# Kernel optimization log

Hardware: AMD Instinct MI355X
Metric: run time of the kernel (lower is better)

## Reference

```python
import jax, jax.numpy as jnp
import numpy as np
from functools import partial

H, W = 96, 96                 # PNet output feature-map size
N = H * W                     # candidate boxes
STRIDE = 2.0
CELL = 12.0
SCALE = 12.0 / 20.0           # net_size / min_face_size (first pyramid level)
CLS_THR = 0.6
NMS_THR1 = 0.5                # per-scale NMS
NMS_THR2 = 0.7                # final NMS


def _iou_matrix(b):
    # b: [N,4] boxes (x1,y1,x2,y2); pixel convention with +1, eps as in source
    x1, y1, x2, y2 = b[:, 0], b[:, 1], b[:, 2], b[:, 3]
    area = (x2 - x1 + 1.0) * (y2 - y1 + 1.0)                      # [N]
    xx1 = jnp.maximum(x1[:, None], x1[None, :])
    yy1 = jnp.maximum(y1[:, None], y1[None, :])
    xx2 = jnp.minimum(x2[:, None], x2[None, :])
    yy2 = jnp.minimum(y2[:, None], y2[None, :])
    w = jnp.maximum(0.0, xx2 - xx1 + 1.0)
    h = jnp.maximum(0.0, yy2 - yy1 + 1.0)
    inter = w * h                                                  # [N,N]
    return inter / (area[:, None] + area[None, :] - inter + 1e-10)


def _greedy_nms(iou, valid, thr):
    # Sequential greedy suppression over score-sorted boxes (rows of iou).
    # A kept box suppresses all LOWER-ranked boxes with IoU > thr.
    n = valid.shape[0]
    ranks = jnp.arange(n)

    def step(suppressed, i):
        kept_i = valid[i] & (~suppressed[i])
        suppressed = suppressed | (kept_i & (iou[i] > thr) & (ranks > i))
        return suppressed, kept_i

    _, keep = jax.lax.scan(step, jnp.zeros(n, dtype=bool), ranks)
    return keep


def _forward(cls_map, reg):
    score = cls_map.reshape(-1)                                    # [N]
    dreg = reg.reshape(-1, 4)                                      # [N,4]
    ys, xs = jnp.meshgrid(jnp.arange(H, dtype=cls_map.dtype),
                          jnp.arange(W, dtype=cls_map.dtype), indexing='ij')
    x1 = jnp.round(STRIDE * xs / SCALE).reshape(-1)
    y1 = jnp.round(STRIDE * ys / SCALE).reshape(-1)
    x2 = jnp.round((STRIDE * xs + CELL) / SCALE).reshape(-1)
    y2 = jnp.round((STRIDE * ys + CELL) / SCALE).reshape(-1)
    boxes = jnp.stack([x1, y1, x2, y2], axis=1)                    # [N,4]

    order = jnp.argsort(-score)                                    # desc by score
    b = boxes[order]
    s = score[order]
    d = dreg[order]
    valid = s > CLS_THR                                            # threshold-gather as mask

    iou = _iou_matrix(b)                                           # [N,N] ~340MB
    keep = _greedy_nms(iou, valid, NMS_THR1)                       # per-scale NMS
    keep = _greedy_nms(iou, keep, NMS_THR2)                        # final NMS

    # box calibration (boxes_c in the source)
    bbw = b[:, 2] - b[:, 0] + 1.0
    bbh = b[:, 3] - b[:, 1] + 1.0
    boxes_c = jnp.stack([b[:, 0] + d[:, 0] * bbw,
                         b[:, 1] + d[:, 1] * bbh,
                         b[:, 2] + d[:, 2] * bbw,
                         b[:, 3] + d[:, 3] * bbh,
                         s], axis=1)                               # [N,5]
    return boxes_c * keep[:, None].astype(boxes_c.dtype)


def setup_inputs() -> dict:
    key = jax.random.key(0)
    k1, k2 = jax.random.split(key)
    cls_map = jax.random.uniform(k1, (H, W), dtype=jnp.float32)        # face prob channel
    reg = 0.1 * jax.random.normal(k2, (H, W, 4), dtype=jnp.float32)    # bbox offsets
    return {"cls_map": cls_map, "reg": reg}


def reference(cls_map, reg):
    return _forward(cls_map, reg)
```

## Files before the change

kernel.cpp:

```cpp
#include <hip/hip_runtime.h>
#include <stdint.h>

#define HH 96
#define WW 96
#define NN (HH*WW)
#define NW 192
#define NMT 24
#define MT 384
#define NKT 9


__device__ __forceinline__ int coord1(int a) { return (10 * a + 1) / 3; }

template<int H, int DJ>
__device__ __forceinline__ unsigned long long shf(unsigned long long S,
                                                  unsigned long long O) {
    if constexpr (DJ == 0) {
        return S;
    } else if constexpr (H == 0) {
        if constexpr (DJ > 0) return (S >> DJ) | (O << (64 - DJ));
        else                  return (S << (-DJ));
    } else {
        if constexpr (DJ > 0) return (S >> DJ);
        else                  return (S << (-DJ)) | (O >> (64 + DJ));
    }
}

template<int H>
__device__ __forceinline__ unsigned long long runfix(
    const int row, const unsigned long long (&Hr)[12],
    volatile unsigned long long* vKs, volatile unsigned long long* vKo,
    volatile unsigned long long* vDs, volatile unsigned long long* vDo,
    unsigned long long myK, unsigned long long myD) {
    const bool okm1 = row >= 1, okp1 = row <= HH - 2;
    const bool okm2 = row >= 2, okp2 = row <= HH - 3;
    for (int iter = 0; iter < 4096; ++iter) {
        if (!~myD) break;
        const unsigned long long D0o  = vDo[row];
        const unsigned long long Dm1s = okm1 ? vDs[row-1] : 0ULL;
        const unsigned long long Dm1o = okm1 ? vDo[row-1] : 0ULL;
        const unsigned long long Dp1s = okp1 ? vDs[row+1] : 0ULL;
        const unsigned long long Dp1o = okp1 ? vDo[row+1] : 0ULL;
        const unsigned long long Dm2  = okm2 ? vDs[row-2] : 0ULL;
        const unsigned long long Dp2  = okp2 ? vDs[row+2] : 0ULL;
        const unsigned long long K0o  = vKo[row];
        const unsigned long long Km1s = okm1 ? vKs[row-1] : 0ULL;
        const unsigned long long Km1o = okm1 ? vKo[row-1] : 0ULL;
        const unsigned long long Kp1s = okp1 ? vKs[row+1] : 0ULL;
        const unsigned long long Kp1o = okp1 ? vKo[row+1] : 0ULL;
        const unsigned long long Km2  = okm2 ? vKs[row-2] : 0ULL;
        const unsigned long long Kp2  = okp2 ? vKs[row+2] : 0ULL;

        unsigned long long supp = 0ULL;
        supp |= Hr[0]  & shf<H,-1>(myK,  K0o);
        supp |= Hr[1]  & shf<H,+1>(myK,  K0o);
        supp |= Hr[2]  & shf<H,-2>(myK,  K0o);
        supp |= Hr[3]  & shf<H,+2>(myK,  K0o);
        supp |= Hr[4]  & Km1s;
        supp |= Hr[5]  & Kp1s;
        supp |= Hr[6]  & Km2;
        supp |= Hr[7]  & Kp2;
        supp |= Hr[8]  & shf<H,-1>(Km1s, Km1o);
        supp |= Hr[9]  & shf<H,+1>(Km1s, Km1o);
        supp |= Hr[10] & shf<H,-1>(Kp1s, Kp1o);
        supp |= Hr[11] & shf<H,+1>(Kp1s, Kp1o);

        unsigned long long alldet = ~0ULL;
        alldet &= ~Hr[0]  | shf<H,-1>(myD,  D0o);
        alldet &= ~Hr[1]  | shf<H,+1>(myD,  D0o);
        alldet &= ~Hr[2]  | shf<H,-2>(myD,  D0o);
        alldet &= ~Hr[3]  | shf<H,+2>(myD,  D0o);
        alldet &= ~Hr[4]  | Dm1s;
        alldet &= ~Hr[5]  | Dp1s;
        alldet &= ~Hr[6]  | Dm2;
        alldet &= ~Hr[7]  | Dp2;
        alldet &= ~Hr[8]  | shf<H,-1>(Dm1s, Dm1o);
        alldet &= ~Hr[9]  | shf<H,+1>(Dm1s, Dm1o);
        alldet &= ~Hr[10] | shf<H,-1>(Dp1s, Dp1o);
        alldet &= ~Hr[11] | shf<H,+1>(Dp1s, Dp1o);

        const unsigned long long U = ~myD;
        myK |= U & alldet & ~supp;
        myD |= U & (supp | alldet);
        vKs[row] = myK;
        vDs[row] = myD;
    }
    return myK;
}

__global__ __launch_bounds__(1024, 1) void kA(const float* __restrict__ cls,
                                              unsigned int* __restrict__ rankp,
                                              unsigned long long* __restrict__ kw) {
    __shared__ __align__(16) float s[NN];
    __shared__ unsigned long long Hh[12][NW];
    __shared__ unsigned long long K2[2][HH], D2[2][HH];
    const int tid = threadIdx.x;
    const int bid = blockIdx.x;

    if (bid != 0) {
        const int rb = bid - 1;
        const int kt = rb % NKT, mt = rb / NKT;
        const int base = mt * MT;
        unsigned long long* sk = (unsigned long long*)s;
        if (tid < MT) {
            const int m = base + tid;
            sk[tid] = ((unsigned long long)__float_as_uint(cls[m]) << 14)
                    | (unsigned long long)(16383 - m);
        }
        __syncthreads();
        const int k = kt * 1024 + tid;
        const unsigned long long kk =
            ((unsigned long long)__float_as_uint(cls[k]) << 14)
          | (unsigned long long)(16383 - k);
        const ulonglong2* sk2 = (const ulonglong2*)sk;
        unsigned c0 = 0, c1 = 0;
        #pragma unroll 4
        for (int m2 = 0; m2 < MT / 2; ++m2) {
            const ulonglong2 v = sk2[m2];
            c0 += (v.x > kk);
            c1 += (v.y > kk);
        }
        rankp[mt * NN + k] = c0 + c1;
        return;
    }

    const int lane = tid & 63;
    const int wave = tid >> 6;
    const int offs_di[12] = {0,0, 0,0, -1,1, -2,2, -1,-1, 1,1};
    const int offs_dj[12] = {-1,1,-2,2,  0,0,  0,0, -1, 1,-1,1};
    for (int i = tid; i < NN/4; i += 1024)
        ((float4*)s)[i] = ((const float4*)cls)[i];
    __syncthreads();
    for (int it = 0; it < 12; ++it) {
        const int w = wave + (it << 4);
        const int row = w >> 1;
        const int col = ((w & 1) << 6) + lane;
        const bool incell = (col < WW);
        const int c = row * WW + col;
        const float sc = incell ? s[c] : 0.0f;
        const unsigned bc = __float_as_uint(sc);
        const int cm3 = col % 3, rm3 = row % 3;
        const unsigned long long dinit = __ballot(!incell || !(sc > 0.6f));
        if (lane == 0) { D2[w & 1][w >> 1] = dinit; K2[w & 1][w >> 1] = 0ULL; }
        #pragma unroll
        for (int e = 0; e < 12; ++e) {
            const int ii = row + offs_di[e], jj = col + offs_dj[e];
            bool geo;
            switch (e) {
                case 2:  geo = (cm3 == 1); break;
                case 3:  geo = (cm3 == 2); break;
                case 6:  geo = (rm3 == 1); break;
                case 7:  geo = (rm3 == 2); break;
                case 8:  geo = !(cm3 == 2 && rm3 == 2); break;
                case 9:  geo = !(cm3 == 1 && rm3 == 2); break;
                case 10: geo = !(cm3 == 2 && rm3 == 1); break;
                case 11: geo = !(cm3 == 1 && rm3 == 1); break;
                default: geo = true;
            }
            const bool tb = (e==0)|(e==2)|(e==4)|(e==6)|(e==8)|(e==9);
            bool hp = false;
            if (incell && geo && ii >= 0 && ii < HH && jj >= 0 && jj < WW) {
                const unsigned bv = __float_as_uint(s[ii * WW + jj]);
                hp = tb ? (bv >= bc) : (bv > bc);
            }
            const unsigned long long m = __ballot(hp);
            if (lane == 0) Hh[e][w] = m;
        }
    }
    __syncthreads();
    if (wave >= 4 || lane >= 48) return;
    const int h2 = wave >> 1;
    const int row = ((wave & 1) * 48) + lane;
    unsigned long long Hr[12];
    #pragma unroll
    for (int e = 0; e < 12; ++e) Hr[e] = Hh[e][row * 2 + h2];
    const unsigned long long myK = K2[h2][row], myD = D2[h2][row];
    unsigned long long fin;
    if (h2 == 0)
        fin = runfix<0>(row, Hr,
                        (volatile unsigned long long*)&K2[0][0],
                        (volatile unsigned long long*)&K2[1][0],
                        (volatile unsigned long long*)&D2[0][0],
                        (volatile unsigned long long*)&D2[1][0], myK, myD);
    else
        fin = runfix<1>(row, Hr,
                        (volatile unsigned long long*)&K2[1][0],
                        (volatile unsigned long long*)&K2[0][0],
                        (volatile unsigned long long*)&D2[1][0],
                        (volatile unsigned long long*)&D2[0][0], myK, myD);
    kw[row * 2 + h2] = fin;
}

__global__ void kout(const float* __restrict__ score, const float* __restrict__ reg,
                     const unsigned int* __restrict__ rankp,
                     const unsigned long long* __restrict__ kw,
                     float* __restrict__ out) {
    const int k = blockIdx.x * 256 + threadIdx.x;
    unsigned r = 0;
    #pragma unroll
    for (int y = 0; y < NMT; ++y) r += rankp[y * NN + k];
    const int j = k % WW, i = k / WW;
    const bool kp = ((kw[i * 2 + (j >> 6)] >> (j & 63)) & 1ULL) != 0ULL;
    const float x1 = (float)coord1(j);
    const float y1 = (float)coord1(i);
    const float4 d = ((const float4*)reg)[k];
    float* o = out + (size_t)r * 5;
    o[0] = kp ? (x1 + d.x * 21.0f) : 0.0f;
    o[1] = kp ? (y1 + d.y * 21.0f) : 0.0f;
    o[2] = kp ? (x1 + 20.0f + d.z * 21.0f) : 0.0f;
    o[3] = kp ? (y1 + 20.0f + d.w * 21.0f) : 0.0f;
    o[4] = kp ? score[k] : 0.0f;
}

extern "C" void kernel_launch(void* const* d_in, const int* in_sizes, int n_in,
                              void* d_out, int out_size, void* d_ws, size_t ws_size,
                              hipStream_t stream) {
    const float* cls = (const float*)d_in[0];
    const float* reg = (const float*)d_in[1];
    float* out = (float*)d_out;
    char* ws = (char*)d_ws;
    unsigned int* rankp = (unsigned int*)(ws);
    unsigned long long* kw = (unsigned long long*)(ws + 884736);

    kA<<<217, 1024, 0, stream>>>(cls, rankp, kw);
    kout<<<36, 256, 0, stream>>>(cls, reg, rankp, kw, out);
}
```

Before: 79.47 us.

## Derive NMS neighbor masks by symmetry, iterate row fixpoint locally, retile rank blocks

The NMS setup now computes only six of the twelve neighbor-precedence bitmasks and derives the remaining six from neighboring rows and words by shifting and complementing. This halves the ballot and LDS work in the single serial block. Each fixpoint iteration applies the horizontal in-row update three times before publishing to shared memory, so fewer cross-row synchronisation rounds are needed. The rank computation is retiled so each thread ranks three keys against a 128-entry tile, using 217 blocks and reusing each LDS load three times. The cost is 72 partial rank slices instead of 24, which kout must sum, plus a larger workspace.

Result: faster. 73.24 us (-7.8%).

```diff
diff --git a/kernel.cpp b/kernel.cpp
--- a/kernel.cpp
+++ b/kernel.cpp
@@ -5,9 +5,10 @@
 #define WW 96
 #define NN (HH*WW)
 #define NW 192
-#define NMT 24
-#define MT 384
-#define NKT 9
+#define NMT 72
+#define MT 128
+#define NKT 3
+#define KW_OFF 2654208
 
 
 __device__ __forceinline__ int coord1(int a) { return (10 * a + 1) / 3; }
@@ -26,14 +27,51 @@
     }
 }
 
+template<int H> struct CM;
+template<> struct CM<0> {
+    static constexpr unsigned long long C1 = 0x2492492492492492ULL;
+    static constexpr unsigned long long C2 = 0x4924924924924924ULL;
+};
+template<> struct CM<1> {
+    static constexpr unsigned long long C1 = 0x9249249249249249ULL;
+    static constexpr unsigned long long C2 = 0x2492492492492492ULL;
+};
+
 template<int H>
 __device__ __forceinline__ unsigned long long runfix(
-    const int row, const unsigned long long (&Hr)[12],
+    const int row, const unsigned long long* Hc,
     volatile unsigned long long* vKs, volatile unsigned long long* vKo,
     volatile unsigned long long* vDs, volatile unsigned long long* vDo,
     unsigned long long myK, unsigned long long myD) {
+    const int w  = row * 2 + H;
+    const int wo = row * 2 + (H ^ 1);
     const bool okm1 = row >= 1, okp1 = row <= HH - 2;
     const bool okm2 = row >= 2, okp2 = row <= HH - 3;
+    const int rm3 = row % 3;
+    unsigned long long Hr[12];
+    {
+        const unsigned long long h0s = Hc[0*NW+w], h0o = Hc[0*NW+wo];
+        const unsigned long long h2s = Hc[1*NW+w], h2o = Hc[1*NW+wo];
+        Hr[0] = h0s;
+        Hr[1] = ~shf<H,1>(h0s, h0o);
+        Hr[2] = h2s;
+        Hr[3] = (~shf<H,2>(h2s, h2o)) & CM<H>::C2;
+        Hr[4] = Hc[2*NW+w];
+        Hr[6] = Hc[3*NW+w];
+        Hr[8] = Hc[4*NW+w];
+        Hr[9] = Hc[5*NW+w];
+        Hr[5] = okp1 ? ~Hc[2*NW+w+2] : 0ULL;
+        Hr[7] = (okp2 && rm3 == 2) ? ~Hc[3*NW+w+4] : 0ULL;
+        if (okp1) {
+            const unsigned long long a8 = Hc[4*NW+w+2], b8 = Hc[4*NW+wo+2];
+            unsigned long long t11 = ~shf<H,1>(a8, b8);
+            const unsigned long long a9 = Hc[5*NW+w+2], b9 = Hc[5*NW+wo+2];
+            unsigned long long t10 = ~shf<H,-1>(a9, b9);
+            if (rm3 == 1) { t11 &= ~CM<H>::C1; t10 &= ~CM<H>::C2; }
+            if constexpr (H == 0) t10 &= ~1ULL;
+            Hr[11] = t11; Hr[10] = t10;
+        } else { Hr[11] = 0ULL; Hr[10] = 0ULL; }
+    }
     for (int iter = 0; iter < 4096; ++iter) {
         if (!~myD) break;
         const unsigned long long D0o  = vDo[row];
@@ -51,37 +89,32 @@
         const unsigned long long Km2  = okm2 ? vKs[row-2] : 0ULL;
         const unsigned long long Kp2  = okp2 ? vKs[row+2] : 0ULL;
 
-        unsigned long long supp = 0ULL;
-        supp |= Hr[0]  & shf<H,-1>(myK,  K0o);
-        supp |= Hr[1]  & shf<H,+1>(myK,  K0o);
-        supp |= Hr[2]  & shf<H,-2>(myK,  K0o);
-        supp |= Hr[3]  & shf<H,+2>(myK,  K0o);
-        supp |= Hr[4]  & Km1s;
-        supp |= Hr[5]  & Kp1s;
-        supp |= Hr[6]  & Km2;
-        supp |= Hr[7]  & Kp2;
-        supp |= Hr[8]  & shf<H,-1>(Km1s, Km1o);
-        supp |= Hr[9]  & shf<H,+1>(Km1s, Km1o);
-        supp |= Hr[10] & shf<H,-1>(Kp1s, Kp1o);
-        supp |= Hr[11] & shf<H,+1>(Kp1s, Kp1o);
-
-        unsigned long long alldet = ~0ULL;
-        alldet &= ~Hr[0]  | shf<H,-1>(myD,  D0o);
-        alldet &= ~Hr[1]  | shf<H,+1>(myD,  D0o);
-        alldet &= ~Hr[2]  | shf<H,-2>(myD,  D0o);
-        alldet &= ~Hr[3]  | shf<H,+2>(myD,  D0o);
-        alldet &= ~Hr[4]  | Dm1s;
-        alldet &= ~Hr[5]  | Dp1s;
-        alldet &= ~Hr[6]  | Dm2;
-        alldet &= ~Hr[7]  | Dp2;
-        alldet &= ~Hr[8]  | shf<H,-1>(Dm1s, Dm1o);
-        alldet &= ~Hr[9]  | shf<H,+1>(Dm1s, Dm1o);
-        alldet &= ~Hr[10] | shf<H,-1>(Dp1s, Dp1o);
-        alldet &= ~Hr[11] | shf<H,+1>(Dp1s, Dp1o);
-
-        const unsigned long long U = ~myD;
-        myK |= U & alldet & ~supp;
-        myD |= U & (supp | alldet);
+        const unsigned long long suppV =
+              (Hr[4]  & Km1s) | (Hr[5] & Kp1s) | (Hr[6] & Km2) | (Hr[7] & Kp2)
+            | (Hr[8]  & shf<H,-1>(Km1s, Km1o)) | (Hr[9]  & shf<H,1>(Km1s, Km1o))
+            | (Hr[10] & shf<H,-1>(Kp1s, Kp1o)) | (Hr[11] & shf<H,1>(Kp1s, Kp1o));
+        unsigned long long alldetV = ~0ULL;
+        alldetV &= ~Hr[4]  | Dm1s;
+        alldetV &= ~Hr[5]  | Dp1s;
+        alldetV &= ~Hr[6]  | Dm2;
+        alldetV &= ~Hr[7]  | Dp2;
+        alldetV &= ~Hr[8]  | shf<H,-1>(Dm1s, Dm1o);
+        alldetV &= ~Hr[9]  | shf<H,1>(Dm1s, Dm1o);
+        alldetV &= ~Hr[10] | shf<H,-1>(Dp1s, Dp1o);
+        alldetV &= ~Hr[11] | shf<H,1>(Dp1s, Dp1o);
+
+        #pragma unroll
+        for (int in = 0; in < 3; ++in) {
+            const unsigned long long supp = suppV
+                | (Hr[0] & shf<H,-1>(myK, K0o)) | (Hr[1] & shf<H,1>(myK, K0o))
+                | (Hr[2] & shf<H,-2>(myK, K0o)) | (Hr[3] & shf<H,2>(myK, K0o));
+            const unsigned long long alldet = alldetV
+                & (~Hr[0] | shf<H,-1>(myD, D0o)) & (~Hr[1] | shf<H,1>(myD, D0o))
+                & (~Hr[2] | shf<H,-2>(myD, D0o)) & (~Hr[3] | shf<H,2>(myD, D0o));
+            const unsigned long long U = ~myD;
+            myK |= U & alldet & ~supp;
+            myD |= U & (supp | alldet);
+        }
         vKs[row] = myK;
         vDs[row] = myD;
     }
@@ -92,7 +125,7 @@
                                               unsigned int* __restrict__ rankp,
                                               unsigned long long* __restrict__ kw) {
     __shared__ __align__(16) float s[NN];
-    __shared__ unsigned long long Hh[12][NW];
+    __shared__ unsigned long long Hc[6][NW];
     __shared__ unsigned long long K2[2][HH], D2[2][HH];
     const int tid = threadIdx.x;
     const int bid = blockIdx.x;
@@ -108,26 +141,32 @@
                     | (unsigned long long)(16383 - m);
         }
         __syncthreads();
-        const int k = kt * 1024 + tid;
-        const unsigned long long kk =
-            ((unsigned long long)__float_as_uint(cls[k]) << 14)
-          | (unsigned long long)(16383 - k);
+        const int k0 = kt * 3072 + tid;
+        const unsigned long long kk0 =
+            ((unsigned long long)__float_as_uint(cls[k0]) << 14)
+          | (unsigned long long)(16383 - k0);
+        const unsigned long long kk1 =
+            ((unsigned long long)__float_as_uint(cls[k0 + 1024]) << 14)
+          | (unsigned long long)(16383 - (k0 + 1024));
+        const unsigned long long kk2 =
+            ((unsigned long long)__float_as_uint(cls[k0 + 2048]) << 14)
+          | (unsigned long long)(16383 - (k0 + 2048));
         const ulonglong2* sk2 = (const ulonglong2*)sk;
-        unsigned c0 = 0, c1 = 0;
-        #pragma unroll 4
+        unsigned a0 = 0, a1 = 0, a2 = 0;
+        #pragma unroll 8
         for (int m2 = 0; m2 < MT / 2; ++m2) {
             const ulonglong2 v = sk2[m2];
-            c0 += (v.x > kk);
-            c1 += (v.y > kk);
+            a0 += (v.x > kk0) + (v.y > kk0);
+            a1 += (v.x > kk1) + (v.y > kk1);
+            a2 += (v.x > kk2) + (v.y > kk2);
         }
-        rankp[mt * NN + k] = c0 + c1;
+        unsigned int* rp = rankp + mt * NN + k0;
+        rp[0] = a0; rp[1024] = a1; rp[2048] = a2;
         return;
     }
 
     const int lane = tid & 63;
     const int wave = tid >> 6;
-    const int offs_di[12] = {0,0, 0,0, -1,1, -2,2, -1,-1, 1,1};
-    const int offs_dj[12] = {-1,1,-2,2,  0,0,  0,0, -1, 1,-1,1};
     for (int i = tid; i < NN/4; i += 1024)
         ((float4*)s)[i] = ((const float4*)cls)[i];
     __syncthreads();
@@ -141,49 +180,39 @@
         const unsigned bc = __float_as_uint(sc);
         const int cm3 = col % 3, rm3 = row % 3;
         const unsigned long long dinit = __ballot(!incell || !(sc > 0.6f));
-        if (lane == 0) { D2[w & 1][w >> 1] = dinit; K2[w & 1][w >> 1] = 0ULL; }
-        #pragma unroll
-        for (int e = 0; e < 12; ++e) {
-            const int ii = row + offs_di[e], jj = col + offs_dj[e];
-            bool geo;
-            switch (e) {
-                case 2:  geo = (cm3 == 1); break;
-                case 3:  geo = (cm3 == 2); break;
-                case 6:  geo = (rm3 == 1); break;
-                case 7:  geo = (rm3 == 2); break;
-                case 8:  geo = !(cm3 == 2 && rm3 == 2); break;
-                case 9:  geo = !(cm3 == 1 && rm3 == 2); break;
-                case 10: geo = !(cm3 == 2 && rm3 == 1); break;
-                case 11: geo = !(cm3 == 1 && rm3 == 1); break;
-                default: geo = true;
-            }
-            const bool tb = (e==0)|(e==2)|(e==4)|(e==6)|(e==8)|(e==9);
-            bool hp = false;
-            if (incell && geo && ii >= 0 && ii < HH && jj >= 0 && jj < WW) {
-                const unsigned bv = __float_as_uint(s[ii * WW + jj]);
-                hp = tb ? (bv >= bc) : (bv > bc);
-            }
-            const unsigned long long m = __ballot(hp);
-            if (lane == 0) Hh[e][w] = m;
-        }
+        if (lane == 0) { D2[w & 1][row] = dinit; K2[w & 1][row] = 0ULL; }
+        const bool okl1 = col >= 1, okl2 = col >= 2, okr1 = col + 1 < WW;
+        const bool oku1 = row >= 1, oku2 = row >= 2;
+        bool hp; unsigned long long m;
+        hp = false; if (incell && okl1) hp = __float_as_uint(s[c-1]) >= bc;
+        m = __ballot(hp); if (lane == 0) Hc[0][w] = m;
+        hp = false; if (incell && okl2 && cm3 == 1) hp = __float_as_uint(s[c-2]) >= bc;
+        m = __ballot(hp); if (lane == 0) Hc[1][w] = m;
+        hp = false; if (incell && oku1) hp = __float_as_uint(s[c-WW]) >= bc;
+        m = __ballot(hp); if (lane == 0) Hc[2][w] = m;
+        hp = false; if (incell && oku2 && rm3 == 1) hp = __float_as_uint(s[c-2*WW]) >= bc;
+        m = __ballot(hp); if (lane == 0) Hc[3][w] = m;
+        hp = false; if (incell && oku1 && okl1 && !(cm3 == 2 && rm3 == 2))
+            hp = __float_as_uint(s[c-WW-1]) >= bc;
+        m = __ballot(hp); if (lane == 0) Hc[4][w] = m;
+        hp = false; if (incell && oku1 && okr1 && !(cm3 == 1 && rm3 == 2))
+            hp = __float_as_uint(s[c-WW+1]) >= bc;
+        m = __ballot(hp); if (lane == 0) Hc[5][w] = m;
     }
     __syncthreads();
     if (wave >= 4 || lane >= 48) return;
     const int h2 = wave >> 1;
     const int row = ((wave & 1) * 48) + lane;
-    unsigned long long Hr[12];
-    #pragma unroll
-    for (int e = 0; e < 12; ++e) Hr[e] = Hh[e][row * 2 + h2];
     const unsigned long long myK = K2[h2][row], myD = D2[h2][row];
     unsigned long long fin;
     if (h2 == 0)
-        fin = runfix<0>(row, Hr,
+        fin = runfix<0>(row, &Hc[0][0],
                         (volatile unsigned long long*)&K2[0][0],
                         (volatile unsigned long long*)&K2[1][0],
                         (volatile unsigned long long*)&D2[0][0],
                         (volatile unsigned long long*)&D2[1][0], myK, myD);
     else
-        fin = runfix<1>(row, Hr,
+        fin = runfix<1>(row, &Hc[0][0],
                         (volatile unsigned long long*)&K2[1][0],
                         (volatile unsigned long long*)&K2[0][0],
                         (volatile unsigned long long*)&D2[1][0],
@@ -220,8 +249,8 @@
     float* out = (float*)d_out;
     char* ws = (char*)d_ws;
     unsigned int* rankp = (unsigned int*)(ws);
-    unsigned long long* kw = (unsigned long long*)(ws + 884736);
-
-    kA<<<217, 1024, 0, stream>>>(cls, rankp, kw);
+    unsigned long long* kw = (unsigned long long*)(ws + KW_OFF);
+
+    kA<<<1 + NKT * NMT, 1024, 0, stream>>>(cls, rankp, kw);
     kout<<<36, 256, 0, stream>>>(cls, reg, rankp, kw, out);
 }
```
